# Optimization experiments

Measured on AMD Instinct MI355X. Metric: run time of the kernel, lower is better.

The kernel has to match this reference:

```python
import jax, jax.numpy as jnp
import numpy as np

B, T, N = 2, 256, 512
H, S, C = 64, 8, 8
DYN = 4


def setup_inputs() -> dict:
    key = jax.random.key(0)
    ks = jax.random.split(key, 12)
    sc = 0.05
    return {
        "x": jax.random.normal(ks[0], (B, T, N), jnp.float32),
        "mask": (jax.random.uniform(ks[1], (B, T, N)) < 0.2).astype(jnp.float32),
        "static_context": jax.random.normal(ks[2], (N, S), jnp.float32),
        "node_coords": jax.random.normal(ks[3], (N, C), jnp.float32),
        "W1": jax.random.normal(ks[4], (DYN + S, H), jnp.float32) * sc,
        "b1": jnp.zeros((H,), jnp.float32),
        "W2": jax.random.normal(ks[5], (H, H), jnp.float32) * sc,
        "b2": jnp.zeros((H,), jnp.float32),
        "We1": jax.random.normal(ks[6], (4 * H, H), jnp.float32) * sc,
        "be1": jnp.zeros((H,), jnp.float32),
        "We2": jax.random.normal(ks[7], (H, 1), jnp.float32) * sc,
        "be2": jnp.zeros((1,), jnp.float32),
        "self_loop_logit": jnp.float32(0.5),
        "prior_strength": jnp.float32(1.0),
        "similarity_strength": jnp.float32(1.0),
        "temperature": jnp.float32(0.7),
    }


def reference(x, mask, static_context, node_coords, W1, b1, W2, b2,
              We1, be1, We2, be2, self_loop_logit, prior_strength,
              similarity_strength, temperature):
    Bv, Tv, Nv = x.shape
    # ---- dynamic per-node context over time ----
    observed = 1.0 - mask                                   # [B,T,N]
    count = jnp.maximum(observed.sum(axis=1), 1.0)          # [B,N]
    mean = (x * observed).sum(axis=1) / count               # [B,N]
    centered = (x - mean[:, None, :]) * observed
    std = jnp.sqrt((centered ** 2).sum(axis=1) / count + 1e-6)
    t_idx = jnp.arange(Tv, dtype=x.dtype)[None, :, None]
    latest = jnp.argmax(t_idx * observed, axis=1)           # [B,N] int
    last = jnp.take_along_axis(x, latest[:, None, :], axis=1)[:, 0, :]
    missing_ratio = mask.mean(axis=1)
    dyn = jnp.stack([mean, std, last, missing_ratio], axis=-1)  # [B,N,4]
    # ---- node encoder ----
    static = jnp.broadcast_to(static_context[None], (Bv, Nv, static_context.shape[-1]))
    feats = jnp.concatenate([dyn, static], axis=-1)
    h = jax.nn.relu(feats @ W1 + b1)
    h = jax.nn.relu(h @ W2 + b2)                            # [B,N,H]
    hn = h / jnp.maximum(jnp.linalg.norm(h, axis=-1, keepdims=True), 1e-12)
    # ---- edge MLP on pair features [h_i, h_j, |h_i-h_j|, h_i*h_j] ----
    # split first-layer weight into the four blocks so h_i/h_j terms are O(N)
    Wi, Wj, Wa, Wp = jnp.split(We1, 4, axis=0)              # each [H,H]
    pre_i = h @ Wi                                          # [B,N,H]
    pre_j = h @ Wj
    hi = h[:, :, None, :]                                   # [B,N,1,H]
    hj = h[:, None, :, :]                                   # [B,1,N,H]
    hidden = jax.nn.relu(pre_i[:, :, None, :] + pre_j[:, None, :, :]
                         + jnp.abs(hi - hj) @ Wa + (hi * hj) @ Wp + be1)
    edge_logits = (hidden @ We2 + be2)[..., 0]              # [B,N,N]
    # ---- cosine similarity + distance prior ----
    cos = jnp.einsum('bnh,bmh->bnm', hn, hn)
    eye = jnp.eye(Nv, dtype=x.dtype)
    off = 1.0 - eye
    diff = node_coords[:, None, :] - node_coords[None, :, :]
    dist = jnp.sqrt(jnp.maximum((diff ** 2).sum(-1), 1e-12))
    prior = (1.0 / (1.0 + dist)) * off                      # [N,N]
    # ---- combine, softmax, symmetrize, row-normalize ----
    logits = (edge_logits * off
              + jax.nn.softplus(prior_strength) * prior[None]
              + jax.nn.softplus(similarity_strength) * (cos * off))
    logits = logits + eye[None] * jax.nn.softplus(self_loop_logit)
    temp = jax.nn.softplus(temperature) + 1e-4
    adj = jax.nn.softmax(logits / temp, axis=-1)
    adj = 0.5 * (adj + jnp.swapaxes(adj, -1, -2))
    adj = adj / jnp.maximum(adj.sum(axis=-1, keepdims=True), 1e-6)
    return adj
```

## Files before the change

kernel.cpp:

```cpp
#include <hip/hip_runtime.h>
#include <hip/hip_bf16.h>
#include <math.h>

#define NB 2
#define NT 256
#define NN 512
#define NH 64
#define NS 8
#define NC 8

#define OFF_H      0
#define OFF_PVEC   65536
#define OFF_HF16   131072
#define OFF_INVN   163840
#define OFF_WA16   164864
#define OFF_WJF    166912
#define OFF_WPF    171008
#define OFF_UNSYM  175104

typedef __attribute__((ext_vector_type(8))) _Float16 h8;
typedef __attribute__((ext_vector_type(2))) __fp16 fp16x2;
typedef __attribute__((ext_vector_type(4))) float f32x4;
typedef __attribute__((ext_vector_type(4))) unsigned u4;
typedef __attribute__((ext_vector_type(2))) unsigned u2;

__device__ __forceinline__ float softplusf(float x){
  if (x > 20.f) return x;
  return log1pf(expf(x));
}

__device__ __forceinline__ unsigned pkh(float a, float b){
  fp16x2 h = __builtin_amdgcn_cvt_pkrtz(a, b);
  return __builtin_bit_cast(unsigned, h);
}

__device__ __forceinline__ float fdot2u(unsigned a, unsigned b, float c){
#if __has_builtin(__builtin_amdgcn_fdot2)
  return __builtin_amdgcn_fdot2(__builtin_bit_cast(fp16x2, a),
                                __builtin_bit_cast(fp16x2, b), c, false);
#else
  fp16x2 av = __builtin_bit_cast(fp16x2, a);
  fp16x2 bv = __builtin_bit_cast(fp16x2, b);
  return fmaf((float)av.x, (float)bv.x, fmaf((float)av.y, (float)bv.y, c));
#endif
}
__device__ __forceinline__ float dot8(u4 a, u4 b, float acc){
  #pragma unroll
  for (int d = 0; d < 4; ++d) acc = fdot2u(a[d], b[d], acc);
  return acc;
}

template<int CTRL>
__device__ __forceinline__ float dpp_addf(float x){
  int xi = __builtin_bit_cast(int, x);
  int yi = __builtin_amdgcn_update_dpp(0, xi, CTRL, 0xF, 0xF, true);
  return x + __builtin_bit_cast(float, yi);
}
__device__ __forceinline__ float row16_sum(float x){
  x = dpp_addf<0xB1>(x);
  x = dpp_addf<0x4E>(x);
  x = dpp_addf<0x141>(x);
  x = dpp_addf<0x140>(x);
  return x;
}

__global__ __launch_bounds__(256) void k_front(
    const float* __restrict__ x, const float* __restrict__ mask,
    const float* __restrict__ sctx,
    const float* __restrict__ W1, const float* __restrict__ b1,
    const float* __restrict__ W2, const float* __restrict__ b2,
    const float* __restrict__ We1, const float* __restrict__ be1,
    float* __restrict__ hg, float* __restrict__ pvec,
    unsigned* __restrict__ hf16, float* __restrict__ invn,
    short* __restrict__ wa16, float* __restrict__ wjf,
    float* __restrict__ wpf){
  int blk = blockIdx.x;
  int tid = threadIdx.x;

  if (blk >= 256){
    int pidx = (blk - 256)*256 + tid;
    int e    = pidx & 7;
    int lane = (pidx >> 3) & 63;
    int frag = (pidx >> 9) & 7;
    int nt = frag & 3, ks = frag >> 2;
    int kg = lane >> 4, q = lane & 15;
    int kk = ks*32 + kg*8 + e;
    int c  = nt*16 + q;
    if (pidx < 4096){
      _Float16 v = (_Float16)We1[(128 + kk)*NH + c];
      wa16[pidx] = __builtin_bit_cast(short, v);
    } else if (pidx < 8192){
      wjf[pidx - 4096] = We1[(64 + kk)*NH + c];
    } else {
      wpf[pidx - 8192] = We1[(192 + kk)*NH + c];
    }
    return;
  }

  int b  = blk >> 7;
  int n0 = (blk & 127) * 4;

  int nl = tid & 3;
  int ts = tid >> 2;
  int n  = n0 + nl;

  float cnt = 0.f, sx = 0.f, sxx = 0.f;
  int lastt = 0;
  for (int t = ts*4; t < ts*4 + 4; ++t){
    int idx = (b*NT + t)*NN + n;
    float xv = x[idx];
    float mv = mask[idx];
    bool obs = (mv < 0.5f);
    if (obs){ cnt += 1.f; sx += xv; sxx += xv*xv; lastt = t; }
  }
  #pragma unroll
  for (int m = 4; m < 64; m <<= 1){
    cnt   += __shfl_xor(cnt,  m);
    sx    += __shfl_xor(sx,   m);
    sxx   += __shfl_xor(sxx,  m);
    lastt  = max(lastt, __shfl_xor(lastt, m));
  }
  int w = tid >> 6;
  __shared__ float r_cnt[4][4], r_sx[4][4], r_sxx[4][4];
  __shared__ int   r_lt[4][4];
  __shared__ float s_dyn[4][4];
  if ((tid & 63) < 4){
    r_cnt[w][nl] = cnt; r_sx[w][nl] = sx; r_sxx[w][nl] = sxx; r_lt[w][nl] = lastt;
  }
  __syncthreads();
  if (tid < 4){
    float c = 0.f, s1 = 0.f, s2 = 0.f; int lt = 0;
    #pragma unroll
    for (int ww = 0; ww < 4; ++ww){
      c  += r_cnt[ww][tid]; s1 += r_sx[ww][tid]; s2 += r_sxx[ww][tid];
      lt  = max(lt, r_lt[ww][tid]);
    }
    float cc   = fmaxf(c, 1.f);
    float mean = s1 / cc;
    float var  = s2 / cc - mean*mean;
    float stdv = sqrtf(fmaxf(var, 0.f) + 1e-6f);
    float last = x[(b*NT + lt)*NN + n0 + tid];
    float mr   = 1.f - c * (1.f/(float)NT);
    s_dyn[tid][0] = mean; s_dyn[tid][1] = stdv; s_dyn[tid][2] = last; s_dyn[tid][3] = mr;
  }
  __syncthreads();

  int c = tid & 63;
  int gn = n0 + w;
  int bn = b*NN + gn;
  __shared__ float s_f[4][12];
  __shared__ float s_h1[4][64];
  __shared__ float s_h2[4][64];

  if (c < 4)       s_f[w][c] = s_dyn[w][c];
  else if (c < 12) s_f[w][c] = sctx[gn*NS + (c-4)];
  __syncthreads();

  float a = b1[c];
  #pragma unroll
  for (int k = 0; k < 12; ++k) a = fmaf(s_f[w][k], W1[k*NH + c], a);
  s_h1[w][c] = fmaxf(a, 0.f);
  __syncthreads();

  float a2 = b2[c];
  #pragma unroll 8
  for (int k = 0; k < 64; ++k) a2 = fmaf(s_h1[w][k], W2[k*NH + c], a2);
  a2 = fmaxf(a2, 0.f);

  float sq = a2*a2;
  #pragma unroll
  for (int m = 1; m < 64; m <<= 1) sq += __shfl_xor(sq, m);
  float inv = 1.f / fmaxf(sqrtf(sq), 1e-12f);

  s_h2[w][c] = a2;
  __syncthreads();

  float pi = be1[c];
  #pragma unroll 8
  for (int k = 0; k < 64; ++k) pi = fmaf(s_h2[w][k], We1[k*NH + c], pi);

  hg  [bn*64 + c] = a2;
  pvec[bn*64 + c] = pi;
  if (c < 32){
    float e0 = s_h2[w][2*c], e1 = s_h2[w][2*c + 1];
    hf16[bn*32 + c] = pkh(e0, e1);
  }
  if (c == 0) invn[bn] = inv;
}

__global__ __launch_bounds__(512, 4) void k_logits(
    const float* __restrict__ hg, const float* __restrict__ pvec,
    const unsigned* __restrict__ hf16, const float* __restrict__ invn,
    const short* __restrict__ wa16, const float* __restrict__ wjf,
    const float* __restrict__ wpf, const float* __restrict__ coords,
    const float* __restrict__ We2, const float* __restrict__ be2,
    const float* __restrict__ s_sl, const float* __restrict__ s_ps,
    const float* __restrict__ s_ss, const float* __restrict__ s_tp,
    float* __restrict__ unsym){
  int blk = blockIdx.x;
  int b  = blk >> 8;
  int ip = (blk & 255) * 2;
  int tid  = threadIdx.x;
  int w    = tid >> 6;
  int lane = tid & 63;
  int q    = lane & 15;
  int kg   = lane >> 4;

  __shared__ __align__(16) float s_hi[2][64];
  __shared__ __align__(16) float s_pri[2][NN];
  __shared__ __align__(16) float s_invn[NN];
  __shared__ __align__(16) float lrow[2][NN];
  __shared__ __align__(16) unsigned lds_wa[2048];
  __shared__ __align__(16) unsigned lds_cw[2][2048];
  __shared__ __align__(16) unsigned s_hj[8][16*34 + 2];
  __shared__ float red[32];

  float spsl = softplusf(s_sl[0]);
  float spps = softplusf(s_ps[0]);
  float spss = softplusf(s_ss[0]);
  float invt = 1.f / (softplusf(s_tp[0]) + 1e-4f);
  float be2v = be2[0];

  if (tid < 128)
    s_hi[tid >> 6][tid & 63] = hg[(b*NN + ip + (tid >> 6))*64 + (tid & 63)];
  {
    int j = tid;
    float4 cj0 = *(const float4*)(coords + j*NC);
    float4 cj1 = *(const float4*)(coords + j*NC + 4);
    #pragma unroll
    for (int r = 0; r < 2; ++r){
      int i = ip + r;
      float4 ci0 = *(const float4*)(coords + i*NC);
      float4 ci1 = *(const float4*)(coords + i*NC + 4);
      float dd = 0.f;
      dd = fmaf(ci0.x-cj0.x, ci0.x-cj0.x, dd);
      dd = fmaf(ci0.y-cj0.y, ci0.y-cj0.y, dd);
      dd = fmaf(ci0.z-cj0.z, ci0.z-cj0.z, dd);
      dd = fmaf(ci0.w-cj0.w, ci0.w-cj0.w, dd);
      dd = fmaf(ci1.x-cj1.x, ci1.x-cj1.x, dd);
      dd = fmaf(ci1.y-cj1.y, ci1.y-cj1.y, dd);
      dd = fmaf(ci1.z-cj1.z, ci1.z-cj1.z, dd);
      dd = fmaf(ci1.w-cj1.w, ci1.w-cj1.w, dd);
      float dist = sqrtf(fmaxf(dd, 1e-12f));
      s_pri[r][j] = (j == i) ? be2v : fmaf(spps, 1.f/(1.f + dist), be2v);
    }
    s_invn[j] = invn[b*NN + j];
  }
  __syncthreads();

  {
    int frag = tid >> 6;
    int l2   = tid & 63;
    const u4* wsrc = (const u4*)wa16;
    *(u4*)&lds_wa[(frag*64 + l2)*4] = wsrc[frag*64 + l2];

    int ch0 = (frag >> 2)*32 + (l2 >> 4)*8;
    const float* wj = wjf + (frag*64 + l2)*8;
    const float* wp = wpf + (frag*64 + l2)*8;
    #pragma unroll
    for (int r = 0; r < 2; ++r){
      u4 u;
      #pragma unroll
      for (int d = 0; d < 4; ++d){
        float v0 = fmaf(s_hi[r][ch0 + 2*d],     wp[2*d],     wj[2*d]);
        float v1 = fmaf(s_hi[r][ch0 + 2*d + 1], wp[2*d + 1], wj[2*d + 1]);
        u[d] = pkh(v0, v1);
      }
      *(u4*)&lds_cw[r][(frag*64 + l2)*4] = u;
    }
  }

  const u4* hfv = (const u4*)hf16;
  u4 hiA[2][2];
  #pragma unroll
  for (int r = 0; r < 2; ++r){
    hiA[r][0] = hfv[(b*NN + ip + r)*8 + kg];
    hiA[r][1] = hfv[(b*NN + ip + r)*8 + kg + 4];
  }

  float pv4[2][4], we2q[4];
  #pragma unroll
  for (int nt = 0; nt < 4; ++nt){
    #pragma unroll
    for (int r = 0; r < 2; ++r)
      pv4[r][nt] = pvec[(b*NN + ip + r)*64 + nt*16 + q];
    we2q[nt] = We2[nt*16 + q];
  }
  float invni[2];
  invni[0] = invn[b*NN + ip];
  invni[1] = invn[b*NN + ip + 1];
  int srcl = (lane & 48) | (((lane >> 4) & 3) << 2) | (lane & 3);
  __syncthreads();

  unsigned* slice = &s_hj[w][0];
  const u4 absm = (u4){0x7fff7fffu, 0x7fff7fffu, 0x7fff7fffu, 0x7fff7fffu};

  #pragma unroll
  for (int s = 0; s < 4; ++s){
    int it = w + s*8;
    int jbase = it * 16;

    {
      int r8 = lane >> 3, c8 = lane & 7;
      u4 g0 = *(const u4*)((const unsigned*)hf16 + (size_t)(b*NN + jbase + r8)*32 + c8*4);
      u4 g1 = *(const u4*)((const unsigned*)hf16 + (size_t)(b*NN + jbase + 8 + r8)*32 + c8*4);
      unsigned* p0 = slice + r8*34 + c8*4;
      unsigned* p1 = slice + (8 + r8)*34 + c8*4;
      u2 t;
      t.x = g0.x; t.y = g0.y; *(u2*)p0 = t;
      t.x = g0.z; t.y = g0.w; *(u2*)(p0 + 2) = t;
      t.x = g1.x; t.y = g1.y; *(u2*)p1 = t;
      t.x = g1.z; t.y = g1.w; *(u2*)(p1 + 2) = t;
    }

    u4 hj0, hj1;
    {
      unsigned* rp = slice + q*34 + kg*4;
      u2 a0 = *(u2*)rp;
      u2 a1 = *(u2*)(rp + 2);
      u2 b0 = *(u2*)(rp + 16);
      u2 b1 = *(u2*)(rp + 18);
      hj0.x = a0.x; hj0.y = a0.y; hj0.z = a1.x; hj0.w = a1.y;
      hj1.x = b0.x; hj1.y = b0.y; hj1.z = b1.x; hj1.w = b1.y;
    }
    h8 hjv0 = __builtin_bit_cast(h8, hj0);
    h8 hjv1 = __builtin_bit_cast(h8, hj1);

    float dotp[2];
    #pragma unroll
    for (int r = 0; r < 2; ++r){
      float d0 = dot8(hiA[r][0], hj0, 0.f);
      dotp[r]  = dot8(hiA[r][1], hj1, d0);
    }

    f32x4 acc[2][4];
    #pragma unroll
    for (int r = 0; r < 2; ++r)
      #pragma unroll
      for (int nt = 0; nt < 4; ++nt)
        acc[r][nt] = (f32x4){pv4[r][nt], pv4[r][nt], pv4[r][nt], pv4[r][nt]};

    #pragma unroll
    for (int nt = 0; nt < 4; ++nt){
      h8 wA0 = __builtin_bit_cast(h8, *(const u4*)&lds_wa[((0*4 + nt)*64 + lane)*4]);
      h8 wA1 = __builtin_bit_cast(h8, *(const u4*)&lds_wa[((1*4 + nt)*64 + lane)*4]);
      #pragma unroll
      for (int r = 0; r < 2; ++r){
        h8 dh0 = __builtin_bit_cast(h8, hiA[r][0]) - hjv0;
        h8 dh1 = __builtin_bit_cast(h8, hiA[r][1]) - hjv1;
        h8 af0 = __builtin_bit_cast(h8, __builtin_bit_cast(u4, dh0) & absm);
        h8 af1 = __builtin_bit_cast(h8, __builtin_bit_cast(u4, dh1) & absm);
        h8 wC0 = __builtin_bit_cast(h8, *(const u4*)&lds_cw[r][((0*4 + nt)*64 + lane)*4]);
        h8 wC1 = __builtin_bit_cast(h8, *(const u4*)&lds_cw[r][((1*4 + nt)*64 + lane)*4]);
        acc[r][nt] = __builtin_amdgcn_mfma_f32_16x16x32_f16(af0, wA0, acc[r][nt], 0, 0, 0);
        acc[r][nt] = __builtin_amdgcn_mfma_f32_16x16x32_f16(af1, wA1, acc[r][nt], 0, 0, 0);
        acc[r][nt] = __builtin_amdgcn_mfma_f32_16x16x32_f16(hjv0, wC0, acc[r][nt], 0, 0, 0);
        acc[r][nt] = __builtin_amdgcn_mfma_f32_16x16x32_f16(hjv1, wC1, acc[r][nt], 0, 0, 0);
      }
    }

    #pragma unroll
    for (int r = 0; r < 2; ++r){
      float part[4] = {0.f, 0.f, 0.f, 0.f};
      #pragma unroll
      for (int nt = 0; nt < 4; ++nt)
        #pragma unroll
        for (int rr = 0; rr < 4; ++rr)
          part[rr] = fmaf(fmaxf(acc[r][nt][rr], 0.f), we2q[nt], part[rr]);
      #pragma unroll
      for (int rr = 0; rr < 4; ++rr) part[rr] = row16_sum(part[rr]);

      float dp = dotp[r];
      dp += __shfl_xor(dp, 16);
      dp += __shfl_xor(dp, 32);
      float dj = __shfl(dp, srcl);

      if (q < 4){
        int j2 = jbase + kg*4 + q;
        float ps2 = part[0];
        ps2 = (q == 1) ? part[1] : ps2;
        ps2 = (q == 2) ? part[2] : ps2;
        ps2 = (q == 3) ? part[3] : ps2;
        float cosv = dj * invni[r] * s_invn[j2];
        lrow[r][j2] = ps2 + s_pri[r][j2] + spss * cosv;
      }
    }
  }
  __syncthreads();

  float va = (tid == ip)     ? spsl : lrow[0][tid];
  float vb = (tid == ip + 1) ? spsl : lrow[1][tid];

  float ma = va, mb = vb;
  #pragma unroll
  for (int msk = 1; msk < 64; msk <<= 1){
    ma = fmaxf(ma, __shfl_xor(ma, msk));
    mb = fmaxf(mb, __shfl_xor(mb, msk));
  }
  if (lane == 0){ red[w] = ma; red[8 + w] = mb; }
  __syncthreads();
  ma = red[0]; mb = red[8];
  #pragma unroll
  for (int ww = 1; ww < 8; ++ww){
    ma = fmaxf(ma, red[ww]);
    mb = fmaxf(mb, red[8 + ww]);
  }

  float ea = expf((va - ma) * invt);
  float eb = expf((vb - mb) * invt);
  float sa = ea, sb = eb;
  #pragma unroll
  for (int msk = 1; msk < 64; msk <<= 1){
    sa += __shfl_xor(sa, msk);
    sb += __shfl_xor(sb, msk);
  }
  if (lane == 0){ red[16 + w] = sa; red[24 + w] = sb; }
  __syncthreads();
  sa = red[16]; sb = red[24];
  #pragma unroll
  for (int ww = 1; ww < 8; ++ww){
    sa += red[16 + ww];
    sb += red[24 + ww];
  }

  unsym[(size_t)(b*NN + ip)*NN + tid]       = ea / sa;
  unsym[(size_t)(b*NN + ip + 1)*NN + tid]   = eb / sb;
}

__global__ __launch_bounds__(256) void k_sym(
    const float* __restrict__ u, float* __restrict__ out){
  int blk = blockIdx.x;
  int b = blk >> 9, i = blk & (NN-1);
  int tid = threadIdx.x;
  const float* urow = u + (size_t)(b*NN + i) * NN;
  float v0, v1, rs;
  {
    int j0 = tid, j1 = tid + 256;
    float a1 = urow[j0];
    float a2 = u[(size_t)(b*NN + j0) * NN + i];
    v0 = 0.5f*(a1 + a2);
    float a3 = urow[j1];
    float a4 = u[(size_t)(b*NN + j1) * NN + i];
    v1 = 0.5f*(a3 + a4);
    rs = v0 + v1;
  }
  int lane = tid & 63, w = tid >> 6;
  #pragma unroll
  for (int msk = 1; msk < 64; msk <<= 1) rs += __shfl_xor(rs, msk);
  __shared__ float red[4];
  if (lane == 0) red[w] = rs;
  __syncthreads();
  rs = red[0] + red[1] + red[2] + red[3];
  float inv = 1.f / fmaxf(rs, 1e-6f);
  float* orow = out + (size_t)(b*NN + i) * NN;
  orow[tid]       = v0 * inv;
  orow[tid + 256] = v1 * inv;
}

extern "C" void kernel_launch(void* const* d_in, const int* in_sizes, int n_in,
                              void* d_out, int out_size, void* d_ws, size_t ws_size,
                              hipStream_t stream){
  const float* x      = (const float*)d_in[0];
  const float* mask   = (const float*)d_in[1];
  const float* sctx   = (const float*)d_in[2];
  const float* coords = (const float*)d_in[3];
  const float* W1     = (const float*)d_in[4];
  const float* b1     = (const float*)d_in[5];
  const float* W2     = (const float*)d_in[6];
  const float* b2     = (const float*)d_in[7];
  const float* We1    = (const float*)d_in[8];
  const float* be1    = (const float*)d_in[9];
  const float* We2    = (const float*)d_in[10];
  const float* be2    = (const float*)d_in[11];
  const float* sl     = (const float*)d_in[12];
  const float* ps     = (const float*)d_in[13];
  const float* ss     = (const float*)d_in[14];
  const float* tp     = (const float*)d_in[15];

  float*    ws    = (float*)d_ws;
  float*    hgp   = ws + OFF_H;
  float*    pvecp = ws + OFF_PVEC;
  unsigned* hf16p = (unsigned*)(ws + OFF_HF16);
  float*    invnp = ws + OFF_INVN;
  short*    wa16p = (short*)(ws + OFF_WA16);
  float*    wjfp  = ws + OFF_WJF;
  float*    wpfp  = ws + OFF_WPF;
  float*    unsym = ws + OFF_UNSYM;
  float*    out   = (float*)d_out;

  k_front <<<304, 256, 0, stream>>>(x, mask, sctx, W1, b1, W2, b2, We1, be1,
                                    hgp, pvecp, hf16p, invnp, wa16p, wjfp, wpfp);
  k_logits<<<NB*NN/2, 512, 0, stream>>>(hgp, pvecp, hf16p, invnp, wa16p, wjfp,
                                        wpfp, coords, We2, be2, sl, ps, ss, tp,
                                        unsym);
  k_sym   <<<NB*NN, 256, 0, stream>>>(unsym, out);
}
```

Before: 43.47 us.

## Prefetch next hj tile into double-buffered LDS and restructure symmetrize kernel

```diff
diff --git a/kernel.cpp b/kernel.cpp
--- a/kernel.cpp
+++ b/kernel.cpp
@@ -212,7 +212,7 @@
   __shared__ __align__(16) float lrow[2][NN];
   __shared__ __align__(16) unsigned lds_wa[2048];
   __shared__ __align__(16) unsigned lds_cw[2][2048];
-  __shared__ __align__(16) unsigned s_hj[8][16*34 + 2];
+  __shared__ __align__(16) unsigned s_hj[8][2][16*34 + 2];
   __shared__ float red[32];
 
   float spsl = softplusf(s_sl[0]);
@@ -290,20 +290,24 @@
   invni[0] = invn[b*NN + ip];
   invni[1] = invn[b*NN + ip + 1];
   int srcl = (lane & 48) | (((lane >> 4) & 3) << 2) | (lane & 3);
-  __syncthreads();
-
-  unsigned* slice = &s_hj[w][0];
+  int r8 = lane >> 3, c8 = lane & 7;
+  __syncthreads();
+
   const u4 absm = (u4){0x7fff7fffu, 0x7fff7fffu, 0x7fff7fffu, 0x7fff7fffu};
 
+  u4 g0, g1;
+  {
+    int jbase = w * 16;
+    g0 = *(const u4*)((const unsigned*)hf16 + (size_t)(b*NN + jbase + r8)*32 + c8*4);
+    g1 = *(const u4*)((const unsigned*)hf16 + (size_t)(b*NN + jbase + 8 + r8)*32 + c8*4);
+  }
+
   #pragma unroll
   for (int s = 0; s < 4; ++s){
-    int it = w + s*8;
-    int jbase = it * 16;
+    int jbase = (w + s*8) * 16;
+    unsigned* slice = &s_hj[w][s & 1][0];
 
     {
-      int r8 = lane >> 3, c8 = lane & 7;
-      u4 g0 = *(const u4*)((const unsigned*)hf16 + (size_t)(b*NN + jbase + r8)*32 + c8*4);
-      u4 g1 = *(const u4*)((const unsigned*)hf16 + (size_t)(b*NN + jbase + 8 + r8)*32 + c8*4);
       unsigned* p0 = slice + r8*34 + c8*4;
       unsigned* p1 = slice + (8 + r8)*34 + c8*4;
       u2 t;
@@ -311,6 +315,11 @@
       t.x = g0.z; t.y = g0.w; *(u2*)(p0 + 2) = t;
       t.x = g1.x; t.y = g1.y; *(u2*)p1 = t;
       t.x = g1.z; t.y = g1.w; *(u2*)(p1 + 2) = t;
+    }
+    if (s < 3){
+      int jn = (w + (s+1)*8) * 16;
+      g0 = *(const u4*)((const unsigned*)hf16 + (size_t)(b*NN + jn + r8)*32 + c8*4);
+      g1 = *(const u4*)((const unsigned*)hf16 + (size_t)(b*NN + jn + 8 + r8)*32 + c8*4);
     }
 
     u4 hj0, hj1;
@@ -427,34 +436,39 @@
   unsym[(size_t)(b*NN + ip + 1)*NN + tid]   = eb / sb;
 }
 
-__global__ __launch_bounds__(256) void k_sym(
+__global__ __launch_bounds__(512) void k_sym(
     const float* __restrict__ u, float* __restrict__ out){
   int blk = blockIdx.x;
-  int b = blk >> 9, i = blk & (NN-1);
-  int tid = threadIdx.x;
-  const float* urow = u + (size_t)(b*NN + i) * NN;
-  float v0, v1, rs;
-  {
-    int j0 = tid, j1 = tid + 256;
-    float a1 = urow[j0];
-    float a2 = u[(size_t)(b*NN + j0) * NN + i];
-    v0 = 0.5f*(a1 + a2);
-    float a3 = urow[j1];
-    float a4 = u[(size_t)(b*NN + j1) * NN + i];
-    v1 = 0.5f*(a3 + a4);
-    rs = v0 + v1;
-  }
+  int b  = blk >> 8;
+  int ip = (blk & 255) * 2;
+  int tid  = threadIdx.x;
   int lane = tid & 63, w = tid >> 6;
-  #pragma unroll
-  for (int msk = 1; msk < 64; msk <<= 1) rs += __shfl_xor(rs, msk);
-  __shared__ float red[4];
-  if (lane == 0) red[w] = rs;
-  __syncthreads();
-  rs = red[0] + red[1] + red[2] + red[3];
-  float inv = 1.f / fmaxf(rs, 1e-6f);
-  float* orow = out + (size_t)(b*NN + i) * NN;
-  orow[tid]       = v0 * inv;
-  orow[tid + 256] = v1 * inv;
+
+  const float* ra = u + (size_t)(b*NN + ip) * NN;
+  const float* rb = u + (size_t)(b*NN + ip + 1) * NN;
+  float2 colv = *(const float2*)(u + (size_t)(b*NN + tid)*NN + ip);
+  float va = 0.5f*(ra[tid] + colv.x);
+  float vb = 0.5f*(rb[tid] + colv.y);
+
+  float sa = va, sb = vb;
+  #pragma unroll
+  for (int msk = 1; msk < 64; msk <<= 1){
+    sa += __shfl_xor(sa, msk);
+    sb += __shfl_xor(sb, msk);
+  }
+  __shared__ float red[16];
+  if (lane == 0){ red[w] = sa; red[8 + w] = sb; }
+  __syncthreads();
+  sa = red[0]; sb = red[8];
+  #pragma unroll
+  for (int ww = 1; ww < 8; ++ww){
+    sa += red[ww];
+    sb += red[8 + ww];
+  }
+  float ia = 1.f / fmaxf(sa, 1e-6f);
+  float ib = 1.f / fmaxf(sb, 1e-6f);
+  out[(size_t)(b*NN + ip)*NN + tid]     = va * ia;
+  out[(size_t)(b*NN + ip + 1)*NN + tid] = vb * ib;
 }
 
 extern "C" void kernel_launch(void* const* d_in, const int* in_sizes, int n_in,
@@ -493,5 +507,5 @@
   k_logits<<<NB*NN/2, 512, 0, stream>>>(hgp, pvecp, hf16p, invnp, wa16p, wjfp,
                                         wpfp, coords, We2, be2, sl, ps, ss, tp,
                                         unsym);
-  k_sym   <<<NB*NN, 256, 0, stream>>>(unsym, out);
-}
+  k_sym   <<<NB*NN/2, 512, 0, stream>>>(unsym, out);
+}
```

Result: no change. 42.87 us (-1.4%).
